# Kernel optimization log

Measured on AMD Instinct MI355X. Metric: run time of the kernel, lower is better.

## Reference

```python
import jax, jax.numpy as jnp
import numpy as np

B, N, DIM = 2, 512, 384
H, SKD, SVD, PKD, PVD, PAIR = 12, 16, 16, 4, 8, 128
EPS = 1e-8
NUM_LOGITS = 3  # scalar + point + pairwise
SCALAR_SCALE = (NUM_LOGITS * SKD) ** -0.5
POINT_SCALE = (NUM_LOGITS * PKD * (9.0 / 2.0)) ** -0.5
PAIR_SCALE = NUM_LOGITS ** -0.5


def setup_inputs() -> dict:
    key = jax.random.key(0)
    ks = jax.random.split(key, 12)
    g = lambda k, shape: jax.random.normal(k, shape, jnp.float32) * 0.02
    return {
        "single_repr": jax.random.normal(ks[0], (B, N, DIM), jnp.float32),
        "pairwise_repr": jax.random.normal(ks[1], (B, N, N, PAIR), jnp.float32),
        "rotations": jax.random.normal(ks[2], (B, N, 3, 3), jnp.float32),
        "translations": jax.random.normal(ks[3], (B, N, 3), jnp.float32),
        "mask": jnp.ones((B, N), dtype=bool),
        "W_sq": g(ks[4], (DIM, H * SKD)),
        "W_sk": g(ks[5], (DIM, H * SKD)),
        "W_sv": g(ks[6], (DIM, H * SVD)),
        "W_pq": g(ks[7], (DIM, H * PKD * 3)),
        "W_pk": g(ks[8], (DIM, H * PKD * 3)),
        "W_pv": g(ks[9], (DIM, H * PVD * 3)),
        "point_weights_raw": jnp.full((H,), float(np.log(np.e - 1.0)), jnp.float32),
        "W_pb": g(ks[10], (PAIR, H)),
        "b_pb": jnp.zeros((H,), jnp.float32),
        "W_out": g(ks[11], (H * (SVD + PVD * 4 + PAIR), DIM)),
        "b_out": jnp.zeros((DIM,), jnp.float32),
    }


def reference(single_repr, pairwise_repr, rotations, translations, mask,
              W_sq, W_sk, W_sv, W_pq, W_pk, W_pv, point_weights_raw,
              W_pb, b_pb, W_out, b_out):
    x = single_repr
    b, n, _ = x.shape
    # scalar q/k/v: b n (h d) -> b n h d
    q_s = (x @ W_sq).reshape(b, n, H, SKD)
    k_s = (x @ W_sk).reshape(b, n, H, SKD)
    v_s = (x @ W_sv).reshape(b, n, H, SVD)
    # point q/k/v: b n (h d c) -> b n h d 3
    q_p = (x @ W_pq).reshape(b, n, H, PKD, 3)
    k_p = (x @ W_pk).reshape(b, n, H, PKD, 3)
    v_p = (x @ W_pv).reshape(b, n, H, PVD, 3)
    # rotate points into global frame and translate
    t = translations[:, :, None, None, :]  # b n 1 1 3
    rot = lambda p: jnp.einsum('bnhdc,bncr->bnhdr', p, rotations) + t
    q_p, k_p, v_p = rot(q_p), rot(k_p), rot(v_p)

    # scalar attention logits  [b h i j]
    logits = jnp.einsum('bihd,bjhd->bhij', q_s, k_s) * SCALAR_SCALE
    # pairwise bias  [b i j h] -> [b h i j]
    pair_bias = pairwise_repr @ W_pb + b_pb
    logits = logits + jnp.transpose(pair_bias, (0, 3, 1, 2)) * PAIR_SCALE
    # point distance logits
    diff = q_p[:, :, None] - k_p[:, None]        # b i j h d 3
    dist = jnp.sum(diff * diff, axis=(-1, -2))   # b i j h
    pw = jax.nn.softplus(point_weights_raw)      # h
    logits = logits - 0.5 * jnp.transpose(dist, (0, 3, 1, 2)) * pw[None, :, None, None] * POINT_SCALE

    m2 = mask[:, :, None] & mask[:, None, :]     # b i j
    logits = jnp.where(m2[:, None], logits, -jnp.finfo(logits.dtype).max)
    attn = jax.nn.softmax(logits, axis=-1)       # b h i j

    res_s = jnp.einsum('bhij,bjhd->bihd', attn, v_s).reshape(b, n, H * SVD)
    res_pair = jnp.einsum('bhij,bijd->bihd', attn, pairwise_repr).reshape(b, n, H * PAIR)
    res_p = jnp.einsum('bhij,bjhdc->bihdc', attn, v_p)
    # rotate back into local frame (apply R^T after subtracting translation)
    res_p = jnp.einsum('bnhdc,bnrc->bnhdr', res_p - t, rotations)
    res_norm = jnp.sqrt(jnp.sum(res_p * res_p, axis=-1) + EPS)  # b n h d

    results = jnp.concatenate([
        res_s,
        res_p.reshape(b, n, H * PVD * 3),
        res_norm.reshape(b, n, H * PVD),
        res_pair,
    ], axis=-1)
    return results @ W_out + b_out
```

## Files before the change

### kernel.cpp

```cpp
#include <hip/hip_runtime.h>
#include <math.h>

#define NB 2
#define NN 512
#define DIMX 384
#define NH 12

#define PCOLS 1152
#define OFF_QS 0
#define OFF_KS 192
#define OFF_VS 384
#define OFF_QP 576
#define OFF_KP 720
#define OFF_VP 864

#define RCOLS 2112
#define ROFF_S 0
#define ROFF_P 192
#define ROFF_NRM 480
#define ROFF_PAIR 576

#define SCALAR_SCALE 0.14433756729740643f
#define POINT_SCALE  0.13608276348795434f
#define PAIR_SCALE   0.57735026918962576f

__global__ __launch_bounds__(256) void k_proj(
    const float* __restrict__ x,
    const float* __restrict__ Wsq, const float* __restrict__ Wsk,
    const float* __restrict__ Wsv, const float* __restrict__ Wpq,
    const float* __restrict__ Wpk, const float* __restrict__ Wpv,
    float* __restrict__ proj)
{
    __shared__ float xs[384 * 36];
    const int t = threadIdx.x;
    const int row0 = blockIdx.y * 32;
    for (int idx = t; idx < 32 * 384; idx += 256) {
        int k = idx % 384, r = idx / 384;
        xs[k * 36 + r] = x[(size_t)(row0 + r) * DIMX + k];
    }
    __syncthreads();

    const int cl = t & 63;
    const int rg = t >> 6;
    const int c = blockIdx.x * 64 + cl;
    const float* W; int wld, lc;
    if (c < 192)      { W = Wsq; wld = 192; lc = c; }
    else if (c < 384) { W = Wsk; wld = 192; lc = c - 192; }
    else if (c < 576) { W = Wsv; wld = 192; lc = c - 384; }
    else if (c < 720) { W = Wpq; wld = 144; lc = c - 576; }
    else if (c < 864) { W = Wpk; wld = 144; lc = c - 720; }
    else              { W = Wpv; wld = 288; lc = c - 864; }
    const float* wp = W + lc;

    float acc[8];
    #pragma unroll
    for (int r = 0; r < 8; ++r) acc[r] = 0.f;
    const int r0 = rg * 8;
    for (int k = 0; k < 384; ++k) {
        float w = wp[(size_t)k * wld];
        float4 a0 = *(const float4*)&xs[k * 36 + r0];
        float4 a1 = *(const float4*)&xs[k * 36 + r0 + 4];
        acc[0] += a0.x * w; acc[1] += a0.y * w; acc[2] += a0.z * w; acc[3] += a0.w * w;
        acc[4] += a1.x * w; acc[5] += a1.y * w; acc[6] += a1.z * w; acc[7] += a1.w * w;
    }
    #pragma unroll
    for (int r = 0; r < 8; ++r)
        proj[(size_t)(row0 + r0 + r) * PCOLS + c] = acc[r];
}

__global__ void k_rot(const float* __restrict__ rotm, const float* __restrict__ trans,
                      float* __restrict__ proj)
{
    int tid = blockIdx.x * 256 + threadIdx.x;
    if (tid >= NB * NN * NH * 16) return;
    int slot = tid & 15;
    int rest = tid >> 4;
    int h = rest % NH;
    int n = rest / NH;
    int col;
    if (slot < 4)      col = OFF_QP + h * 12 + slot * 3;
    else if (slot < 8) col = OFF_KP + h * 12 + (slot - 4) * 3;
    else               col = OFF_VP + h * 24 + (slot - 8) * 3;
    float* p = proj + (size_t)n * PCOLS + col;
    float p0 = p[0], p1 = p[1], p2 = p[2];
    const float* R = rotm + (size_t)n * 9;
    const float* T = trans + (size_t)n * 3;
    float o0 = p0 * R[0] + p1 * R[3] + p2 * R[6] + T[0];
    float o1 = p0 * R[1] + p1 * R[4] + p2 * R[7] + T[1];
    float o2 = p0 * R[2] + p1 * R[5] + p2 * R[8] + T[2];
    p[0] = o0; p[1] = o1; p[2] = o2;
}

__global__ __launch_bounds__(512, 4) void k_attn(
    const float* __restrict__ pair, const float* __restrict__ rotm,
    const float* __restrict__ trans, const float* __restrict__ pwraw,
    const float* __restrict__ Wpb, const float* __restrict__ bpb,
    const float* __restrict__ proj, float* __restrict__ results)
{
    __shared__ float l_att[2 * 12 * 512];
    __shared__ float l_wpbT[12 * 128];
    __shared__ float l_q[2][192];
    __shared__ float l_qp[2][144];
    __shared__ float l_pw[12];
    __shared__ float l_bpb[12];
    __shared__ float l_resp[2][288];

    const int t = threadIdx.x;
    const int b = blockIdx.x >> 8;
    const int ip = (blockIdx.x & 255) * 2;
    const float* projb = proj + (size_t)b * NN * PCOLS;

    for (int idx = t; idx < 1536; idx += 512) {
        int dd = idx / 12, h = idx % 12;
        l_wpbT[h * 128 + dd] = Wpb[idx];
    }
    for (int idx = t; idx < 2 * 192; idx += 512) {
        int i = idx / 192, cc = idx % 192;
        l_q[i][cc] = projb[(size_t)(ip + i) * PCOLS + OFF_QS + cc];
    }
    if (t < 2 * 144) {
        int i = t / 144, cc = t % 144;
        l_qp[i][cc] = projb[(size_t)(ip + i) * PCOLS + OFF_QP + cc];
    }
    if (t < 12) { l_pw[t] = log1pf(expf(pwraw[t])); l_bpb[t] = bpb[t]; }
    __syncthreads();

    {
        const int j = t;
        const float* pr0 = pair + (((size_t)(b * NN + ip)) * NN + j) * 128;
        const float* pr1 = pr0 + (size_t)NN * 128;
        float bias0[12], bias1[12];
        #pragma unroll
        for (int h = 0; h < 12; ++h) { bias0[h] = 0.f; bias1[h] = 0.f; }
        const float4* wpb4 = (const float4*)l_wpbT;
        #pragma unroll 2
        for (int dg = 0; dg < 32; ++dg) {
            float4 p0 = ((const float4*)pr0)[dg];
            float4 p1 = ((const float4*)pr1)[dg];
            #pragma unroll
            for (int h = 0; h < 12; ++h) {
                float4 w = wpb4[h * 32 + dg];
                bias0[h] += p0.x * w.x + p0.y * w.y + p0.z * w.z + p0.w * w.w;
                bias1[h] += p1.x * w.x + p1.y * w.y + p1.z * w.z + p1.w * w.w;
            }
        }
        const float* kr = projb + (size_t)j * PCOLS;
        #pragma unroll 2
        for (int h = 0; h < 12; ++h) {
            const float4* ks4 = (const float4*)(kr + OFF_KS + h * 16);
            const float4* q0 = (const float4*)(&l_q[0][h * 16]);
            const float4* q1 = (const float4*)(&l_q[1][h * 16]);
            float s0 = 0.f, s1 = 0.f;
            #pragma unroll
            for (int u = 0; u < 4; ++u) {
                float4 kv = ks4[u]; float4 a = q0[u]; float4 cq = q1[u];
                s0 += a.x * kv.x + a.y * kv.y + a.z * kv.z + a.w * kv.w;
                s1 += cq.x * kv.x + cq.y * kv.y + cq.z * kv.z + cq.w * kv.w;
            }
            const float4* kp4 = (const float4*)(kr + OFF_KP + h * 12);
            const float4* e0 = (const float4*)(&l_qp[0][h * 12]);
            const float4* e1 = (const float4*)(&l_qp[1][h * 12]);
            float d0 = 0.f, d1 = 0.f;
            #pragma unroll
            for (int u = 0; u < 3; ++u) {
                float4 kv = kp4[u]; float4 a = e0[u]; float4 cq = e1[u];
                float x0 = a.x - kv.x, x1 = a.y - kv.y, x2 = a.z - kv.z, x3 = a.w - kv.w;
                d0 += x0 * x0 + x1 * x1 + x2 * x2 + x3 * x3;
                float y0 = cq.x - kv.x, y1 = cq.y - kv.y, y2 = cq.z - kv.z, y3 = cq.w - kv.w;
                d1 += y0 * y0 + y1 * y1 + y2 * y2 + y3 * y3;
            }
            float pwc = 0.5f * POINT_SCALE * l_pw[h];
            float lg0 = s0 * SCALAR_SCALE + (bias0[h] + l_bpb[h]) * PAIR_SCALE - pwc * d0;
            float lg1 = s1 * SCALAR_SCALE + (bias1[h] + l_bpb[h]) * PAIR_SCALE - pwc * d1;
            l_att[h * 512 + j] = lg0;
            l_att[(12 + h) * 512 + j] = lg1;
        }
    }
    __syncthreads();

    {
        const int w = t >> 6, lane = t & 63;
        for (int row = w; row < 24; row += 8) {
            float* ptr = l_att + row * 512;
            float v[8]; float m = -1e30f;
            #pragma unroll
            for (int q = 0; q < 8; ++q) { v[q] = ptr[lane + 64 * q]; m = fmaxf(m, v[q]); }
            #pragma unroll
            for (int s = 32; s; s >>= 1) m = fmaxf(m, __shfl_xor(m, s));
            float sum = 0.f;
            #pragma unroll
            for (int q = 0; q < 8; ++q) { v[q] = __expf(v[q] - m); sum += v[q]; }
            #pragma unroll
            for (int s = 32; s; s >>= 1) sum += __shfl_xor(sum, s);
            float inv = 1.0f / sum;
            #pragma unroll
            for (int q = 0; q < 8; ++q) ptr[lane + 64 * q] = v[q] * inv;
        }
    }
    __syncthreads();

    float rp00 = 0, rp01 = 0, rp02 = 0, rp10 = 0, rp11 = 0, rp12 = 0;
    const int dd = t & 127, g = t >> 7;
    const float* pb0 = pair + ((size_t)(b * NN + ip)) * NN * 128 + dd;
    const float* pb1 = pb0 + (size_t)NN * 128;
    float accs0 = 0.f, accs1 = 0.f;
    int vcol = -1; int hx = 0;
    if (t < 192)      { hx = t >> 4; vcol = OFF_VS + hx * 16 + (t & 15); }
    else if (t < 480) { int o = t - 192; hx = o / 24; vcol = OFF_VP + hx * 24 + (o % 24); }
    const float* at0a = l_att + g * 512;
    const float* at0b = l_att + (g + 4) * 512;
    const float* at0c = l_att + (g + 8) * 512;
    const float* at1a = l_att + (12 + g) * 512;
    const float* at1b = l_att + (12 + g + 4) * 512;
    const float* at1c = l_att + (12 + g + 8) * 512;
    const float* atx0 = l_att + hx * 512;
    const float* atx1 = l_att + (12 + hx) * 512;

    #pragma unroll 2
    for (int j4 = 0; j4 < 512; j4 += 4) {
        float p00 = pb0[(size_t)(j4 + 0) * 128];
        float p01 = pb0[(size_t)(j4 + 1) * 128];
        float p02 = pb0[(size_t)(j4 + 2) * 128];
        float p03 = pb0[(size_t)(j4 + 3) * 128];
        float p10 = pb1[(size_t)(j4 + 0) * 128];
        float p11 = pb1[(size_t)(j4 + 1) * 128];
        float p12 = pb1[(size_t)(j4 + 2) * 128];
        float p13 = pb1[(size_t)(j4 + 3) * 128];
        float4 a;
        a = *(const float4*)(at0a + j4); rp00 += a.x * p00 + a.y * p01 + a.z * p02 + a.w * p03;
        a = *(const float4*)(at0b + j4); rp01 += a.x * p00 + a.y * p01 + a.z * p02 + a.w * p03;
        a = *(const float4*)(at0c + j4); rp02 += a.x * p00 + a.y * p01 + a.z * p02 + a.w * p03;
        a = *(const float4*)(at1a + j4); rp10 += a.x * p10 + a.y * p11 + a.z * p12 + a.w * p13;
        a = *(const float4*)(at1b + j4); rp11 += a.x * p10 + a.y * p11 + a.z * p12 + a.w * p13;
        a = *(const float4*)(at1c + j4); rp12 += a.x * p10 + a.y * p11 + a.z * p12 + a.w * p13;
        if (vcol >= 0) {
            float v0 = projb[(size_t)(j4 + 0) * PCOLS + vcol];
            float v1 = projb[(size_t)(j4 + 1) * PCOLS + vcol];
            float v2 = projb[(size_t)(j4 + 2) * PCOLS + vcol];
            float v3 = projb[(size_t)(j4 + 3) * PCOLS + vcol];
            a = *(const float4*)(atx0 + j4); accs0 += a.x * v0 + a.y * v1 + a.z * v2 + a.w * v3;
            a = *(const float4*)(atx1 + j4); accs1 += a.x * v0 + a.y * v1 + a.z * v2 + a.w * v3;
        }
    }

    float* res0 = results + (size_t)(b * NN + ip) * RCOLS;
    float* res1 = res0 + RCOLS;
    res0[ROFF_PAIR + g * 128 + dd]       = rp00;
    res0[ROFF_PAIR + (g + 4) * 128 + dd] = rp01;
    res0[ROFF_PAIR + (g + 8) * 128 + dd] = rp02;
    res1[ROFF_PAIR + g * 128 + dd]       = rp10;
    res1[ROFF_PAIR + (g + 4) * 128 + dd] = rp11;
    res1[ROFF_PAIR + (g + 8) * 128 + dd] = rp12;
    if (t < 192) {
        res0[ROFF_S + t] = accs0;
        res1[ROFF_S + t] = accs1;
    } else if (t < 480) {
        l_resp[0][t - 192] = accs0;
        l_resp[1][t - 192] = accs1;
    }
    __syncthreads();

    if (t < 192) {
        int i = t / 96, o = t % 96;
        int h = o >> 3, p = o & 7;
        const float* v = &l_resp[i][h * 24 + p * 3];
        int n = b * NN + ip + i;
        const float* R = rotm + (size_t)n * 9;
        const float* T = trans + (size_t)n * 3;
        float c0 = v[0] - T[0], c1 = v[1] - T[1], c2 = v[2] - T[2];
        float o0 = c0 * R[0] + c1 * R[1] + c2 * R[2];
        float o1 = c0 * R[3] + c1 * R[4] + c2 * R[5];
        float o2 = c0 * R[6] + c1 * R[7] + c2 * R[8];
        float* rr = results + (size_t)n * RCOLS;
        rr[ROFF_P + h * 24 + p * 3 + 0] = o0;
        rr[ROFF_P + h * 24 + p * 3 + 1] = o1;
        rr[ROFF_P + h * 24 + p * 3 + 2] = o2;
        rr[ROFF_NRM + h * 8 + p] = sqrtf(o0 * o0 + o1 * o1 + o2 * o2 + 1e-8f);
    }
}

__global__ void k_init_out(const float* __restrict__ bout, float* __restrict__ out)
{
    int tid = blockIdx.x * 256 + threadIdx.x;
    if (tid < NB * NN * DIMX) out[tid] = bout[tid % DIMX];
}

__global__ __launch_bounds__(384) void k_out(
    const float* __restrict__ res, const float* __restrict__ Wout,
    float* __restrict__ out)
{
    __shared__ float a_lds[132 * 16];
    const int t = threadIdx.x;
    const int row0 = blockIdx.x * 16;
    const int ks = blockIdx.y;
    float acc[16];
    #pragma unroll
    for (int r = 0; r < 16; ++r) acc[r] = 0.f;

    for (int chunk = 0; chunk < 4; ++chunk) {
        const int k0 = ks * 528 + chunk * 132;
        for (int idx = t; idx < 16 * 132; idx += 384) {
            int kk = idx % 132, r = idx / 132;
            a_lds[kk * 16 + r] = res[(size_t)(row0 + r) * RCOLS + k0 + kk];
        }
        __syncthreads();
        for (int kk = 0; kk < 132; ++kk) {
            float w = Wout[(size_t)(k0 + kk) * DIMX + t];
            float4 a0 = *(const float4*)&a_lds[kk * 16 + 0];
            float4 a1 = *(const float4*)&a_lds[kk * 16 + 4];
            float4 a2 = *(const float4*)&a_lds[kk * 16 + 8];
            float4 a3 = *(const float4*)&a_lds[kk * 16 + 12];
            acc[0]  += a0.x * w; acc[1]  += a0.y * w; acc[2]  += a0.z * w; acc[3]  += a0.w * w;
            acc[4]  += a1.x * w; acc[5]  += a1.y * w; acc[6]  += a1.z * w; acc[7]  += a1.w * w;
            acc[8]  += a2.x * w; acc[9]  += a2.y * w; acc[10] += a2.z * w; acc[11] += a2.w * w;
            acc[12] += a3.x * w; acc[13] += a3.y * w; acc[14] += a3.z * w; acc[15] += a3.w * w;
        }
        __syncthreads();
    }
    #pragma unroll
    for (int r = 0; r < 16; ++r)
        atomicAdd(&out[(size_t)(row0 + r) * DIMX + t], acc[r]);
}

extern "C" void kernel_launch(void* const* d_in, const int* in_sizes, int n_in,
                              void* d_out, int out_size, void* d_ws, size_t ws_size,
                              hipStream_t stream)
{
    const float* x      = (const float*)d_in[0];
    const float* pair   = (const float*)d_in[1];
    const float* rotm   = (const float*)d_in[2];
    const float* trans  = (const float*)d_in[3];
    const float* Wsq    = (const float*)d_in[5];
    const float* Wsk    = (const float*)d_in[6];
    const float* Wsv    = (const float*)d_in[7];
    const float* Wpq    = (const float*)d_in[8];
    const float* Wpk    = (const float*)d_in[9];
    const float* Wpv    = (const float*)d_in[10];
    const float* pwraw  = (const float*)d_in[11];
    const float* Wpb    = (const float*)d_in[12];
    const float* bpb    = (const float*)d_in[13];
    const float* Wout   = (const float*)d_in[14];
    const float* bout   = (const float*)d_in[15];
    float* out = (float*)d_out;

    float* proj    = (float*)d_ws;
    float* results = proj + (size_t)NB * NN * PCOLS;

    k_proj<<<dim3(18, 32), 256, 0, stream>>>(x, Wsq, Wsk, Wsv, Wpq, Wpk, Wpv, proj);
    k_rot<<<(NB * NN * NH * 16 + 255) / 256, 256, 0, stream>>>(rotm, trans, proj);
    k_init_out<<<(NB * NN * DIMX + 255) / 256, 256, 0, stream>>>(bout, out);
    k_attn<<<NB * NN / 2, 512, 0, stream>>>(pair, rotm, trans, pwraw, Wpb, bpb, proj, results);
    k_out<<<dim3(64, 4), 384, 0, stream>>>(results, Wout, out);
}
```

Baseline: 779.8 us.

## Process one query row per attention block and split output GEMM K further

The attention kernel now handles one query row per block instead of two. That doubles the grid to 1024 blocks, halves LDS use (attention scratch drops from 48KB to 24KB), and raises the launch-bounds occupancy hint to 8. This trades the reuse of K/V projection loads across two rows for more blocks and higher occupancy. The output GEMM also splits K into 8 slices instead of 4, which gives more blocks and more atomic/partial accumulations.

```diff
diff --git a/kernel.cpp b/kernel.cpp
--- a/kernel.cpp
+++ b/kernel.cpp
@@ -91,96 +91,87 @@
     p[0] = o0; p[1] = o1; p[2] = o2;
 }
 
-__global__ __launch_bounds__(512, 4) void k_attn(
+__global__ __launch_bounds__(512, 8) void k_attn(
     const float* __restrict__ pair, const float* __restrict__ rotm,
     const float* __restrict__ trans, const float* __restrict__ pwraw,
     const float* __restrict__ Wpb, const float* __restrict__ bpb,
     const float* __restrict__ proj, float* __restrict__ results)
 {
-    __shared__ float l_att[2 * 12 * 512];
+    __shared__ float l_att[12 * 512];
     __shared__ float l_wpbT[12 * 128];
-    __shared__ float l_q[2][192];
-    __shared__ float l_qp[2][144];
+    __shared__ float l_q[192];
+    __shared__ float l_qp[144];
     __shared__ float l_pw[12];
     __shared__ float l_bpb[12];
-    __shared__ float l_resp[2][288];
+    __shared__ float l_resp[288];
 
     const int t = threadIdx.x;
-    const int b = blockIdx.x >> 8;
-    const int ip = (blockIdx.x & 255) * 2;
+    const int b = blockIdx.x >> 9;
+    const int ii = blockIdx.x & 511;
     const float* projb = proj + (size_t)b * NN * PCOLS;
+    const size_t rowbase = ((size_t)(b * NN + ii)) * NN * 128;
 
     for (int idx = t; idx < 1536; idx += 512) {
         int dd = idx / 12, h = idx % 12;
         l_wpbT[h * 128 + dd] = Wpb[idx];
     }
-    for (int idx = t; idx < 2 * 192; idx += 512) {
-        int i = idx / 192, cc = idx % 192;
-        l_q[i][cc] = projb[(size_t)(ip + i) * PCOLS + OFF_QS + cc];
-    }
-    if (t < 2 * 144) {
-        int i = t / 144, cc = t % 144;
-        l_qp[i][cc] = projb[(size_t)(ip + i) * PCOLS + OFF_QP + cc];
-    }
-    if (t < 12) { l_pw[t] = log1pf(expf(pwraw[t])); l_bpb[t] = bpb[t]; }
+    if (t < 192) {
+        l_q[t] = projb[(size_t)ii * PCOLS + OFF_QS + t];
+    } else if (t < 336) {
+        l_qp[t - 192] = projb[(size_t)ii * PCOLS + OFF_QP + (t - 192)];
+    } else if (t < 348) {
+        int h = t - 336;
+        l_pw[h] = log1pf(expf(pwraw[h]));
+        l_bpb[h] = bpb[h];
+    }
     __syncthreads();
 
     {
         const int j = t;
-        const float* pr0 = pair + (((size_t)(b * NN + ip)) * NN + j) * 128;
-        const float* pr1 = pr0 + (size_t)NN * 128;
-        float bias0[12], bias1[12];
+        const float* pr0 = pair + rowbase + (size_t)j * 128;
+        float bias[12];
         #pragma unroll
-        for (int h = 0; h < 12; ++h) { bias0[h] = 0.f; bias1[h] = 0.f; }
+        for (int h = 0; h < 12; ++h) bias[h] = 0.f;
         const float4* wpb4 = (const float4*)l_wpbT;
         #pragma unroll 2
         for (int dg = 0; dg < 32; ++dg) {
             float4 p0 = ((const float4*)pr0)[dg];
-            float4 p1 = ((const float4*)pr1)[dg];
             #pragma unroll
             for (int h = 0; h < 12; ++h) {
                 float4 w = wpb4[h * 32 + dg];
-                bias0[h] += p0.x * w.x + p0.y * w.y + p0.z * w.z + p0.w * w.w;
-                bias1[h] += p1.x * w.x + p1.y * w.y + p1.z * w.z + p1.w * w.w;
+                bias[h] += p0.x * w.x + p0.y * w.y + p0.z * w.z + p0.w * w.w;
             }
         }
         const float* kr = projb + (size_t)j * PCOLS;
         #pragma unroll 2
         for (int h = 0; h < 12; ++h) {
             const float4* ks4 = (const float4*)(kr + OFF_KS + h * 16);
-            const float4* q0 = (const float4*)(&l_q[0][h * 16]);
-            const float4* q1 = (const float4*)(&l_q[1][h * 16]);
-            float s0 = 0.f, s1 = 0.f;
+            const float4* q0 = (const float4*)(&l_q[h * 16]);
+            float s0 = 0.f;
             #pragma unroll
             for (int u = 0; u < 4; ++u) {
-                float4 kv = ks4[u]; float4 a = q0[u]; float4 cq = q1[u];
+                float4 kv = ks4[u]; float4 a = q0[u];
                 s0 += a.x * kv.x + a.y * kv.y + a.z * kv.z + a.w * kv.w;
-                s1 += cq.x * kv.x + cq.y * kv.y + cq.z * kv.z + cq.w * kv.w;
             }
             const float4* kp4 = (const float4*)(kr + OFF_KP + h * 12);
-            const float4* e0 = (const float4*)(&l_qp[0][h * 12]);
-            const float4* e1 = (const float4*)(&l_qp[1][h * 12]);
-            float d0 = 0.f, d1 = 0.f;
+            const float4* e0 = (const float4*)(&l_qp[h * 12]);
+            float d0 = 0.f;
             #pragma unroll
             for (int u = 0; u < 3; ++u) {
-                float4 kv = kp4[u]; float4 a = e0[u]; float4 cq = e1[u];
+                float4 kv = kp4[u]; float4 a = e0[u];
                 float x0 = a.x - kv.x, x1 = a.y - kv.y, x2 = a.z - kv.z, x3 = a.w - kv.w;
                 d0 += x0 * x0 + x1 * x1 + x2 * x2 + x3 * x3;
-                float y0 = cq.x - kv.x, y1 = cq.y - kv.y, y2 = cq.z - kv.z, y3 = cq.w - kv.w;
-                d1 += y0 * y0 + y1 * y1 + y2 * y2 + y3 * y3;
             }
             float pwc = 0.5f * POINT_SCALE * l_pw[h];
-            float lg0 = s0 * SCALAR_SCALE + (bias0[h] + l_bpb[h]) * PAIR_SCALE - pwc * d0;
-            float lg1 = s1 * SCALAR_SCALE + (bias1[h] + l_bpb[h]) * PAIR_SCALE - pwc * d1;
-            l_att[h * 512 + j] = lg0;
-            l_att[(12 + h) * 512 + j] = lg1;
+            l_att[h * 512 + j] =
+                s0 * SCALAR_SCALE + (bias[h] + l_bpb[h]) * PAIR_SCALE - pwc * d0;
         }
     }
     __syncthreads();
 
     {
         const int w = t >> 6, lane = t & 63;
-        for (int row = w; row < 24; row += 8) {
+        for (int row = w; row < 12; row += 8) {
             float* ptr = l_att + row * 512;
             float v[8]; float m = -1e30f;
             #pragma unroll
@@ -199,72 +190,53 @@
     }
     __syncthreads();
 
-    float rp00 = 0, rp01 = 0, rp02 = 0, rp10 = 0, rp11 = 0, rp12 = 0;
+    float rp0 = 0.f, rp1 = 0.f, rp2 = 0.f;
     const int dd = t & 127, g = t >> 7;
-    const float* pb0 = pair + ((size_t)(b * NN + ip)) * NN * 128 + dd;
-    const float* pb1 = pb0 + (size_t)NN * 128;
-    float accs0 = 0.f, accs1 = 0.f;
+    const float* pb = pair + rowbase + dd;
+    float accs = 0.f;
     int vcol = -1; int hx = 0;
     if (t < 192)      { hx = t >> 4; vcol = OFF_VS + hx * 16 + (t & 15); }
     else if (t < 480) { int o = t - 192; hx = o / 24; vcol = OFF_VP + hx * 24 + (o % 24); }
-    const float* at0a = l_att + g * 512;
-    const float* at0b = l_att + (g + 4) * 512;
-    const float* at0c = l_att + (g + 8) * 512;
-    const float* at1a = l_att + (12 + g) * 512;
-    const float* at1b = l_att + (12 + g + 4) * 512;
-    const float* at1c = l_att + (12 + g + 8) * 512;
-    const float* atx0 = l_att + hx * 512;
-    const float* atx1 = l_att + (12 + hx) * 512;
+    const float* ata = l_att + g * 512;
+    const float* atb = l_att + (g + 4) * 512;
+    const float* atc = l_att + (g + 8) * 512;
+    const float* atx = l_att + hx * 512;
 
     #pragma unroll 2
     for (int j4 = 0; j4 < 512; j4 += 4) {
-        float p00 = pb0[(size_t)(j4 + 0) * 128];
-        float p01 = pb0[(size_t)(j4 + 1) * 128];
-        float p02 = pb0[(size_t)(j4 + 2) * 128];
-        float p03 = pb0[(size_t)(j4 + 3) * 128];
-        float p10 = pb1[(size_t)(j4 + 0) * 128];
-        float p11 = pb1[(size_t)(j4 + 1) * 128];
-        float p12 = pb1[(size_t)(j4 + 2) * 128];
-        float p13 = pb1[(size_t)(j4 + 3) * 128];
+        float p0 = pb[(size_t)(j4 + 0) * 128];
+        float p1 = pb[(size_t)(j4 + 1) * 128];
+        float p2 = pb[(size_t)(j4 + 2) * 128];
+        float p3 = pb[(size_t)(j4 + 3) * 128];
         float4 a;
-        a = *(const float4*)(at0a + j4); rp00 += a.x * p00 + a.y * p01 + a.z * p02 + a.w * p03;
-        a = *(const float4*)(at0b + j4); rp01 += a.x * p00 + a.y * p01 + a.z * p02 + a.w * p03;
-        a = *(const float4*)(at0c + j4); rp02 += a.x * p00 + a.y * p01 + a.z * p02 + a.w * p03;
-        a = *(const float4*)(at1a + j4); rp10 += a.x * p10 + a.y * p11 + a.z * p12 + a.w * p13;
-        a = *(const float4*)(at1b + j4); rp11 += a.x * p10 + a.y * p11 + a.z * p12 + a.w * p13;
-        a = *(const float4*)(at1c + j4); rp12 += a.x * p10 + a.y * p11 + a.z * p12 + a.w * p13;
+        a = *(const float4*)(ata + j4); rp0 += a.x * p0 + a.y * p1 + a.z * p2 + a.w * p3;
+        a = *(const float4*)(atb + j4); rp1 += a.x * p0 + a.y * p1 + a.z * p2 + a.w * p3;
+        a = *(const float4*)(atc + j4); rp2 += a.x * p0 + a.y * p1 + a.z * p2 + a.w * p3;
         if (vcol >= 0) {
             float v0 = projb[(size_t)(j4 + 0) * PCOLS + vcol];
             float v1 = projb[(size_t)(j4 + 1) * PCOLS + vcol];
             float v2 = projb[(size_t)(j4 + 2) * PCOLS + vcol];
             float v3 = projb[(size_t)(j4 + 3) * PCOLS + vcol];
-            a = *(const float4*)(atx0 + j4); accs0 += a.x * v0 + a.y * v1 + a.z * v2 + a.w * v3;
-            a = *(const float4*)(atx1 + j4); accs1 += a.x * v0 + a.y * v1 + a.z * v2 + a.w * v3;
-        }
-    }
-
-    float* res0 = results + (size_t)(b * NN + ip) * RCOLS;
-    float* res1 = res0 + RCOLS;
-    res0[ROFF_PAIR + g * 128 + dd]       = rp00;
-    res0[ROFF_PAIR + (g + 4) * 128 + dd] = rp01;
-    res0[ROFF_PAIR + (g + 8) * 128 + dd] = rp02;
-    res1[ROFF_PAIR + g * 128 + dd]       = rp10;
-    res1[ROFF_PAIR + (g + 4) * 128 + dd] = rp11;
-    res1[ROFF_PAIR + (g + 8) * 128 + dd] = rp12;
+            a = *(const float4*)(atx + j4);
+            accs += a.x * v0 + a.y * v1 + a.z * v2 + a.w * v3;
+        }
+    }
+
+    float* res0 = results + (size_t)(b * NN + ii) * RCOLS;
+    res0[ROFF_PAIR + g * 128 + dd]       = rp0;
+    res0[ROFF_PAIR + (g + 4) * 128 + dd] = rp1;
+    res0[ROFF_PAIR + (g + 8) * 128 + dd] = rp2;
     if (t < 192) {
-        res0[ROFF_S + t] = accs0;
-        res1[ROFF_S + t] = accs1;
+        res0[ROFF_S + t] = accs;
     } else if (t < 480) {
-        l_resp[0][t - 192] = accs0;
-        l_resp[1][t - 192] = accs1;
-    }
-    __syncthreads();
-
-    if (t < 192) {
-        int i = t / 96, o = t % 96;
-        int h = o >> 3, p = o & 7;
-        const float* v = &l_resp[i][h * 24 + p * 3];
-        int n = b * NN + ip + i;
+        l_resp[t - 192] = accs;
+    }
+    __syncthreads();
+
+    if (t < 96) {
+        int h = t >> 3, p = t & 7;
+        const float* v = &l_resp[h * 24 + p * 3];
+        int n = b * NN + ii;
         const float* R = rotm + (size_t)n * 9;
         const float* T = trans + (size_t)n * 3;
         float c0 = v[0] - T[0], c1 = v[1] - T[1], c2 = v[2] - T[2];
@@ -297,8 +269,8 @@
     #pragma unroll
     for (int r = 0; r < 16; ++r) acc[r] = 0.f;
 
-    for (int chunk = 0; chunk < 4; ++chunk) {
-        const int k0 = ks * 528 + chunk * 132;
+    for (int chunk = 0; chunk < 2; ++chunk) {
+        const int k0 = ks * 264 + chunk * 132;
         for (int idx = t; idx < 16 * 132; idx += 384) {
             int kk = idx % 132, r = idx / 132;
             a_lds[kk * 16 + r] = res[(size_t)(row0 + r) * RCOLS + k0 + kk];
@@ -349,6 +321,6 @@
     k_proj<<<dim3(18, 32), 256, 0, stream>>>(x, Wsq, Wsk, Wsv, Wpq, Wpk, Wpv, proj);
     k_rot<<<(NB * NN * NH * 16 + 255) / 256, 256, 0, stream>>>(rotm, trans, proj);
     k_init_out<<<(NB * NN * DIMX + 255) / 256, 256, 0, stream>>>(bout, out);
-    k_attn<<<NB * NN / 2, 512, 0, stream>>>(pair, rotm, trans, pwraw, Wpb, bpb, proj, results);
-    k_out<<<dim3(64, 4), 384, 0, stream>>>(results, Wout, out);
-}
+    k_attn<<<NB * NN, 512, 0, stream>>>(pair, rotm, trans, pwraw, Wpb, bpb, proj, results);
+    k_out<<<dim3(64, 8), 384, 0, stream>>>(results, Wout, out);
+}
```

Result: slower. 859.9 us (+10.3%).
